# Optimization experiments

Hardware: AMD Instinct MI355X
Metric: run time of the kernel (lower is better)

## Reference

```python
import jax, jax.numpy as jnp
import numpy as np

VOCAB = 32000
DIM = 1024
DEPTH = 4
SEQ = 512
HEADS = 16
NMB = 4
MAXMEM = NMB * SEQ  # 2048
RAMP = 128
COEF = 1e-06
B = 4
DH = DIM // HEADS


def _ln(x, g, b):
    mu = jnp.mean(x, axis=-1, keepdims=True)
    v = jnp.mean((x - mu) ** 2, axis=-1, keepdims=True)
    return (x - mu) / jnp.sqrt(v + 1e-5) * g + b


def setup_inputs() -> dict:
    key = jax.random.key(0)
    ks = jax.random.split(key, 24)
    s = 0.02
    inp = {
        'tokens': jax.random.randint(ks[0], (B, SEQ), 0, VOCAB),
        'mems': jax.random.normal(ks[1], (DEPTH, B, MAXMEM, DIM), jnp.float32) * s,
        'times': jax.random.randint(ks[2], (DEPTH, MAXMEM), 0, 4096, dtype=jnp.int32),
        'token_emb': jax.random.normal(ks[3], (VOCAB, DIM), jnp.float32) * s,
        'expire_W': jax.random.normal(ks[4], (DEPTH, DIM), jnp.float32) * s,
        'expire_b': jnp.full((DEPTH,), -float(MAXMEM), jnp.float32),  # torch init constant
        'ln1_g': jnp.ones((DEPTH, DIM), jnp.float32),
        'ln1_b': jnp.zeros((DEPTH, DIM), jnp.float32),
        'Wq': jax.random.normal(ks[5], (DEPTH, DIM, DIM), jnp.float32) * s,
        'Wkv': jax.random.normal(ks[6], (DEPTH, DIM, 2 * DIM), jnp.float32) * s,
        'Wo': jax.random.normal(ks[7], (DEPTH, DIM, DIM), jnp.float32) * s,
        'bo': jnp.zeros((DEPTH, DIM), jnp.float32),
        'ln2_g': jnp.ones((DEPTH, DIM), jnp.float32),
        'ln2_b': jnp.zeros((DEPTH, DIM), jnp.float32),
        'W1': jax.random.normal(ks[8], (DEPTH, DIM, 4 * DIM), jnp.float32) * s,
        'b1': jnp.zeros((DEPTH, 4 * DIM), jnp.float32),
        'W2': jax.random.normal(ks[9], (DEPTH, 4 * DIM, DIM), jnp.float32) * s,
        'b2': jnp.zeros((DEPTH, DIM), jnp.float32),
        'logits_W': jax.random.normal(ks[10], (DIM, VOCAB), jnp.float32) * s,
        'logits_b': jnp.zeros((VOCAB,), jnp.float32),
    }
    return inp


def reference(tokens, mems, times, token_emb, expire_W, expire_b, ln1_g, ln1_b,
              Wq, Wkv, Wo, bo, ln2_g, ln2_b, W1, b1, W2, b2, logits_W, logits_b):
    n, M = SEQ, MAXMEM
    scale = DH ** -0.5
    x = token_emb[tokens]  # (B, n, DIM)
    # causal mask over concat(mem, x): query i may attend key j iff j <= i + M
    causal = jnp.triu(jnp.ones((n, M + n), bool), k=M + 1)  # True = masked
    aux = jnp.float32(0.0)
    new_mems, new_times = [], []
    tnew = jnp.arange(n - 1, -1, -1, dtype=times.dtype)
    for d in range(DEPTH):
        mem = mems[d]                       # (B, M, DIM)
        t = times[d].astype(jnp.float32)    # (M,)
        hidden = x
        # --- expire span: per-memory-slot soft retention mask ---
        exps = jax.nn.sigmoid(mem @ expire_W[d] + expire_b[d]) * M  # (B, M)
        r = exps[:, None, None, :] - t[None, None, None, :]          # (B,1,1,M)
        r = jnp.pad(r, ((0, 0), (0, 0), (0, 0), (0, n)), constant_values=1.0)
        emask = jnp.clip(r / RAMP + 1.0, 0.0, 1.0)                   # (B,1,1,M+n)
        # --- pre-norm causal attention over concat(mem, x_normed) ---
        xn = _ln(x, ln1_g[d], ln1_b[d])
        q = (xn @ Wq[d]).reshape(B, n, HEADS, DH).transpose(0, 2, 1, 3)
        ctx = jnp.concatenate([mem, xn], axis=1)                     # (B, M+n, DIM)
        kv = ctx @ Wkv[d]
        k = kv[..., :DIM].reshape(B, M + n, HEADS, DH).transpose(0, 2, 1, 3)
        v = kv[..., DIM:].reshape(B, M + n, HEADS, DH).transpose(0, 2, 1, 3)
        dots = jnp.einsum('bhid,bhjd->bhij', q, k) * scale
        dots = jnp.where(causal, -jnp.inf, dots)
        attn = jax.nn.softmax(dots, axis=-1) * emask
        out = jnp.einsum('bhij,bhjd->bhid', attn, v)
        out = out.transpose(0, 2, 1, 3).reshape(B, n, DIM)
        x = out @ Wo[d] + bo[d] + x
        # --- pre-norm FFN ---
        xn2 = _ln(x, ln2_g[d], ln2_b[d])
        x = jax.nn.gelu(xn2 @ W1[d] + b1[d], approximate=False) @ W2[d] + b2[d] + x
        aux = aux + (exps / SEQ).sum() * COEF
        # --- memory bookkeeping (detached) ---
        new_mems.append(jax.lax.stop_gradient(
            jnp.concatenate([mem, hidden], axis=1)[:, -M:]))
        new_times.append(jnp.concatenate([times[d] + n, tnew])[-M:])
    logits = x @ logits_W + logits_b
    return (logits, jnp.stack(new_mems), jnp.stack(new_times), aux)
```

## Files before the change

### kernel.cpp

```cpp
#include <hip/hip_runtime.h>
#include <cmath>

#define DIMC   1024
#define SEQC   512
#define BC     4
#define MC     2048
#define CTXC   2560
#define HEADSC 16
#define DHC    64
#define VOCABC 32000

using short8 = __attribute__((ext_vector_type(8))) short;
using f32x4  = __attribute__((ext_vector_type(4))) float;
using u16x4  = __attribute__((ext_vector_type(4))) unsigned short;
using u16x8  = __attribute__((ext_vector_type(8))) unsigned short;

__device__ __forceinline__ unsigned short f2bf(float f) {
    unsigned u = __float_as_uint(f);
    unsigned r = (u + 0x7fffu + ((u >> 16) & 1u)) >> 16;
    return (unsigned short)r;
}

__device__ __forceinline__ void glds16(const unsigned short* g, char* l) {
    __builtin_amdgcn_global_load_lds(
        (const __attribute__((address_space(1))) void*)g,
        (__attribute__((address_space(3))) void*)l, 16, 0, 0);
}

__global__ __launch_bounds__(256) void embed_kernel(const int* __restrict__ tokens,
                                                    const float* __restrict__ emb,
                                                    float* __restrict__ x) {
    int row = blockIdx.x;
    int tok = tokens[row];
    const float4 v = *(const float4*)(emb + (size_t)tok * DIMC + threadIdx.x * 4);
    *(float4*)(x + (size_t)row * DIMC + threadIdx.x * 4) = v;
}

__global__ __launch_bounds__(256) void times_init_kernel(const int* __restrict__ times,
                                                         float* __restrict__ out_times,
                                                         float* __restrict__ aux) {
    int i = blockIdx.x * 256 + threadIdx.x;
    if (i == 0) aux[0] = 0.0f;
    if (i < 4 * MC) {
        int d = i >> 11, m = i & (MC - 1);
        out_times[i] = (m < MC - SEQC) ? (float)(times[d * MC + SEQC + m] + SEQC)
                                       : (float)(MC - 1 - m);
    }
}

#define PREP_MEM 8192
#define PREP_XC  10240
#define PREP_LN  12288
#define PREP_TOT 24576
__global__ __launch_bounds__(256) void prep_kernel(
    const float* __restrict__ mem_d, const float* __restrict__ x,
    const float* __restrict__ eW, const float* __restrict__ eb,
    float* __restrict__ exps, float* __restrict__ aux,
    unsigned short* __restrict__ mem_b, float* __restrict__ out_mems_d,
    const float* __restrict__ g1, const float* __restrict__ b1v,
    unsigned short* __restrict__ xn_b,
    const float* __restrict__ Wq, const float* __restrict__ Wkv,
    const float* __restrict__ Wo, const float* __restrict__ W1,
    const float* __restrict__ W2,
    unsigned short* __restrict__ wq_t, unsigned short* __restrict__ wkv_t,
    unsigned short* __restrict__ wo_t, unsigned short* __restrict__ w1_t,
    unsigned short* __restrict__ w2_t) {
    __shared__ float sh[1056];
    const int bid = blockIdx.x, tid = threadIdx.x;
    if (bid < PREP_MEM) {
        int row = bid;
        int m = row & 2047, b = row >> 11;
        const float4 v = *(const float4*)(mem_d + (size_t)row * DIMC + tid * 4);
        const float4 w = *(const float4*)(eW + tid * 4);
        float s = v.x * w.x + v.y * w.y + v.z * w.z + v.w * w.w;
        for (int off = 32; off; off >>= 1) s += __shfl_down(s, off, 64);
        int wid = tid >> 6, lane = tid & 63;
        if (lane == 0) sh[wid] = s;
        u16x4 o = { f2bf(v.x), f2bf(v.y), f2bf(v.z), f2bf(v.w) };
        *(u16x4*)(mem_b + (size_t)row * DIMC + tid * 4) = o;
        if (m >= SEQC)
            *(float4*)(out_mems_d + ((size_t)(b * MC + m - SEQC)) * DIMC + tid * 4) = v;
        __syncthreads();
        if (tid == 0) {
            float z = sh[0] + sh[1] + sh[2] + sh[3] + eb[0];
            float e = (float)MC / (1.0f + expf(-z));
            exps[row] = e;
            atomicAdd(aux, e * (1e-6f / (float)SEQC));
        }
    } else if (bid < PREP_XC) {
        int r = bid - PREP_MEM;
        int b = r >> 9, i = r & 511;
        const float4 v = *(const float4*)(x + (size_t)r * DIMC + tid * 4);
        *(float4*)(out_mems_d + ((size_t)(b * MC + MC - SEQC + i)) * DIMC + tid * 4) = v;
    } else if (bid < PREP_LN) {
        int row = bid - PREP_XC;
        const float4 v = *(const float4*)(x + (size_t)row * DIMC + tid * 4);
        float s = v.x + v.y + v.z + v.w;
        float q = v.x * v.x + v.y * v.y + v.z * v.z + v.w * v.w;
        for (int off = 32; off; off >>= 1) {
            s += __shfl_down(s, off, 64);
            q += __shfl_down(q, off, 64);
        }
        int wid = tid >> 6, lane = tid & 63;
        if (lane == 0) { sh[wid] = s; sh[4 + wid] = q; }
        __syncthreads();
        if (tid == 0) {
            float S = sh[0] + sh[1] + sh[2] + sh[3];
            float Q = sh[4] + sh[5] + sh[6] + sh[7];
            float mu = S / DIMC;
            float var = Q / DIMC - mu * mu;
            sh[8] = mu;
            sh[9] = rsqrtf(var + 1e-5f);
        }
        __syncthreads();
        float mu = sh[8], rstd = sh[9];
        const float4 gg = *(const float4*)(g1 + tid * 4);
        const float4 bb = *(const float4*)(b1v + tid * 4);
        u16x4 o = { f2bf((v.x - mu) * rstd * gg.x + bb.x),
                    f2bf((v.y - mu) * rstd * gg.y + bb.y),
                    f2bf((v.z - mu) * rstd * gg.z + bb.z),
                    f2bf((v.w - mu) * rstd * gg.w + bb.w) };
        *(u16x4*)(xn_b + (size_t)row * DIMC + tid * 4) = o;
    } else {
        int t = bid - PREP_LN;
        const float* W; unsigned short* Wt; int K, N, tx, ty;
        if (t < 1024)      { W = Wq;  Wt = wq_t;  K = 1024; N = 1024; tx = t & 31;  ty = t >> 5; }
        else if (t < 3072) { int u = t - 1024; W = Wkv; Wt = wkv_t; K = 1024; N = 2048; tx = u & 63;  ty = u >> 6; }
        else if (t < 4096) { int u = t - 3072; W = Wo;  Wt = wo_t;  K = 1024; N = 1024; tx = u & 31;  ty = u >> 5; }
        else if (t < 8192) { int u = t - 4096; W = W1;  Wt = w1_t;  K = 1024; N = 4096; tx = u & 127; ty = u >> 7; }
        else               { int u = t - 8192; W = W2;  Wt = w2_t;  K = 4096; N = 1024; tx = u & 31;  ty = u >> 5; }
        int n0 = tx * 32, k0 = ty * 32;
        int r = tid >> 3, c = (tid & 7) * 4;
        const float4 v = *(const float4*)(W + (size_t)(k0 + r) * N + n0 + c);
        sh[r * 33 + c] = v.x; sh[r * 33 + c + 1] = v.y;
        sh[r * 33 + c + 2] = v.z; sh[r * 33 + c + 3] = v.w;
        __syncthreads();
        u16x4 o = { f2bf(sh[(c + 0) * 33 + r]), f2bf(sh[(c + 1) * 33 + r]),
                    f2bf(sh[(c + 2) * 33 + r]), f2bf(sh[(c + 3) * 33 + r]) };
        *(u16x4*)(Wt + (size_t)(n0 + r) * K + k0 + c) = o;
    }
}

__global__ __launch_bounds__(64) void compact_kernel(
    const float* __restrict__ exps, const int* __restrict__ times_d,
    int* __restrict__ cidx, float* __restrict__ em_c, int* __restrict__ cnt) {
    int b = blockIdx.x, lane = threadIdx.x;
    int c = 0;
    for (int it = 0; it < 32; ++it) {
        int j = it * 64 + lane;
        float e = exps[b * MC + j];
        float rr = (e - (float)times_d[j]) * (1.0f / 128.0f) + 1.0f;
        float em = fminf(fmaxf(rr, 0.0f), 1.0f);
        unsigned long long mk = __ballot(em > 0.0f);
        int pos = c + __popcll(mk & ((1ull << lane) - 1ull));
        if (em > 0.0f) {
            cidx[b * 2048 + pos] = j;
            em_c[b * 2048 + pos] = em;
        }
        c += __popcll(mk);
    }
    int padded = (c + 63) & ~63;
    for (int p = c + lane; p < padded; p += 64) {
        cidx[b * 2048 + p] = 0;
        em_c[b * 2048 + p] = 0.0f;
    }
    if (lane == 0) cnt[b] = padded >> 6;
}

__global__ __launch_bounds__(256) void ln_kernel(const float* __restrict__ in,
                                                 const float* __restrict__ g,
                                                 const float* __restrict__ b,
                                                 unsigned short* __restrict__ outb) {
    int row = blockIdx.x;
    int tid = threadIdx.x;
    const float4 v = *(const float4*)(in + (size_t)row * DIMC + tid * 4);
    float s = v.x + v.y + v.z + v.w;
    float q = v.x * v.x + v.y * v.y + v.z * v.z + v.w * v.w;
    for (int off = 32; off; off >>= 1) {
        s += __shfl_down(s, off, 64);
        q += __shfl_down(q, off, 64);
    }
    __shared__ float ss[4], sq[4];
    int wid = tid >> 6, lane = tid & 63;
    if (lane == 0) { ss[wid] = s; sq[wid] = q; }
    __syncthreads();
    if (tid == 0) {
        float S = ss[0] + ss[1] + ss[2] + ss[3];
        float Q = sq[0] + sq[1] + sq[2] + sq[3];
        float mu = S / DIMC;
        float var = Q / DIMC - mu * mu;
        ss[0] = mu;
        sq[0] = rsqrtf(var + 1e-5f);
    }
    __syncthreads();
    float mu = ss[0], rstd = sq[0];
    const float4 gg = *(const float4*)(g + tid * 4);
    const float4 bb = *(const float4*)(b + tid * 4);
    u16x4 o = { f2bf((v.x - mu) * rstd * gg.x + bb.x),
                f2bf((v.y - mu) * rstd * gg.y + bb.y),
                f2bf((v.z - mu) * rstd * gg.z + bb.z),
                f2bf((v.w - mu) * rstd * gg.w + bb.w) };
    *(u16x4*)(outb + (size_t)row * DIMC + tid * 4) = o;
}

__global__ __launch_bounds__(256) void wt_kernel(const float* __restrict__ W,
                                                 unsigned short* __restrict__ Wt,
                                                 int K, int N) {
    __shared__ float t[32][33];
    int tid = threadIdx.x;
    int n0 = blockIdx.x * 32, k0 = blockIdx.y * 32;
    int r = tid >> 3, c = (tid & 7) * 4;
    const float4 v = *(const float4*)(W + (size_t)(k0 + r) * N + n0 + c);
    t[r][c] = v.x; t[r][c + 1] = v.y; t[r][c + 2] = v.z; t[r][c + 3] = v.w;
    __syncthreads();
    u16x4 o = { f2bf(t[c + 0][r]), f2bf(t[c + 1][r]),
                f2bf(t[c + 2][r]), f2bf(t[c + 3][r]) };
    *(u16x4*)(Wt + (size_t)(n0 + r) * K + k0 + c) = o;
}

__global__ __launch_bounds__(256) void vt_kernel(const unsigned short* __restrict__ kvb,
                                                 unsigned short* __restrict__ vT) {
    __shared__ unsigned short t[64][72];
    int jt = blockIdx.x, dt = blockIdx.y, b = blockIdx.z;
    int j0 = MC + jt * 64;
    int tid = threadIdx.x;
    int r = tid >> 3, c = (tid & 7) * 8;
    #pragma unroll
    for (int p = 0; p < 2; ++p) {
        u16x8 v = *(const u16x8*)(kvb + ((size_t)(b * CTXC + j0 + r + p * 32)) * 2048
                                  + 1024 + dt * 64 + c);
        *(u16x8*)&t[r + p * 32][c] = v;
    }
    __syncthreads();
    #pragma unroll
    for (int p = 0; p < 2; ++p) {
        int dr = r + p * 32;
        u16x8 o = { t[c + 0][dr], t[c + 1][dr], t[c + 2][dr], t[c + 3][dr],
                    t[c + 4][dr], t[c + 5][dr], t[c + 6][dr], t[c + 7][dr] };
        *(u16x8*)(vT + ((size_t)(b * 1024 + dt * 64 + dr)) * CTXC + j0 + c) = o;
    }
}

__global__ __launch_bounds__(256) void vtc_kernel(const unsigned short* __restrict__ kvb,
                                                  const int* __restrict__ cidx,
                                                  const int* __restrict__ cnt,
                                                  unsigned short* __restrict__ vTc) {
    int ct = blockIdx.x, dt = blockIdx.y, b = blockIdx.z;
    if (ct >= cnt[b]) return;
    __shared__ unsigned short t[64][72];
    int tid = threadIdx.x;
    int r = tid >> 3, c = (tid & 7) * 8;
    #pragma unroll
    for (int p = 0; p < 2; ++p) {
        int row = cidx[b * 2048 + ct * 64 + r + p * 32];
        u16x8 v = *(const u16x8*)(kvb + ((size_t)(b * CTXC + row)) * 2048
                                  + 1024 + dt * 64 + c);
        *(u16x8*)&t[r + p * 32][c] = v;
    }
    __syncthreads();
    #pragma unroll
    for (int p = 0; p < 2; ++p) {
        int dr = r + p * 32;
        u16x8 o = { t[c + 0][dr], t[c + 1][dr], t[c + 2][dr], t[c + 3][dr],
                    t[c + 4][dr], t[c + 5][dr], t[c + 6][dr], t[c + 7][dr] };
        *(u16x8*)(vTc + ((size_t)(b * 1024 + dt * 64 + dr)) * 2048 + ct * 64 + c) = o;
    }
}

template<bool GATHER, bool BIAS, bool GELU, bool RES, int RT>
__device__ __forceinline__ void gemm_body(
    unsigned short* As, unsigned short* Bs,
    const unsigned short* __restrict__ A, const unsigned short* __restrict__ A2,
    const unsigned short* __restrict__ Wt, const float* __restrict__ bias,
    const float* __restrict__ res, float* __restrict__ Cf,
    unsigned short* __restrict__ Cb, int K, int N, int bx, int by) {
    constexpr int MF = RT / 32;
    const int tid = threadIdx.x;
    const int lane = tid & 63, wave = tid >> 6;
    const int row0 = by * RT, col0 = bx * 128;

    const int seg = tid & 3;
    const int rr0 = tid >> 2;
    const unsigned short* arow[RT / 64];
    #pragma unroll
    for (int p = 0; p < RT / 64; ++p) {
        int r = row0 + p * 64 + rr0;
        if (GATHER) {
            int b = r / CTXC, rm = r - b * CTXC;
            arow[p] = (rm < MC) ? A + ((size_t)(b * MC + rm)) * K
                                : A2 + ((size_t)(b * SEQC + rm - MC)) * K;
        } else {
            arow[p] = A + (size_t)r * K;
        }
        arow[p] += seg * 8;
    }
    const unsigned short* brow[2];
    #pragma unroll
    for (int p = 0; p < 2; ++p)
        brow[p] = Wt + (size_t)(col0 + p * 64 + rr0) * K + seg * 8;

    char* lA = (char*)As + (tid & 192) * 16;
    char* lB = (char*)Bs + (tid & 192) * 16;

    auto stage = [&](int k0, int q) {
        char* a = lA + q * (RT * 64);
        glds16(arow[0] + k0, a);
        if (RT == 128) glds16(arow[1] + k0, a + 4096);
        char* bp = lB + q * 8192;
        glds16(brow[0] + k0, bp);
        glds16(brow[1] + k0, bp + 4096);
    };

    f32x4 acc[MF][4] = {};

    const int wr = (wave >> 1) * (RT / 2), wc = (wave & 1) * 64;
    const int fr = lane & 15;
    const int k8 = (lane >> 4) * 8;

    stage(0, 0);
    __syncthreads();
    int cur = 0;
    for (int k0 = 0; k0 < K; k0 += 32) {
        if (k0 + 32 < K) stage(k0 + 32, cur ^ 1);
        const unsigned short* Ar = As + cur * (RT * 32) + (size_t)(wr + fr) * 32 + k8;
        const unsigned short* Br = Bs + cur * (128 * 32) + (size_t)(wc + fr) * 32 + k8;
        short8 a[MF], b[4];
        #pragma unroll
        for (int m = 0; m < MF; ++m) a[m] = *(const short8*)(Ar + m * 16 * 32);
        #pragma unroll
        for (int n = 0; n < 4; ++n) b[n] = *(const short8*)(Br + n * 16 * 32);
        #pragma unroll
        for (int m = 0; m < MF; ++m)
            #pragma unroll
            for (int n = 0; n < 4; ++n)
                acc[m][n] = __builtin_amdgcn_mfma_f32_16x16x32_bf16(a[m], b[n], acc[m][n], 0, 0, 0);
        __syncthreads();
        cur ^= 1;
    }

    const int orow = row0 + wr + (lane >> 4) * 4;
    const int ocol = col0 + wc + fr;
    #pragma unroll
    for (int n = 0; n < 4; ++n) {
        int c = ocol + n * 16;
        float bv = BIAS ? bias[c] : 0.0f;
        #pragma unroll
        for (int m = 0; m < MF; ++m) {
            #pragma unroll
            for (int i = 0; i < 4; ++i) {
                size_t idx = (size_t)(orow + m * 16 + i) * N + c;
                float v = acc[m][n][i] + bv;
                if (GELU) v = 0.5f * v * (1.0f + erff(v * 0.70710678118f));
                if (RES) v += res[idx];
                if (Cf) Cf[idx] = v;
                if (Cb) Cb[idx] = f2bf(v);
            }
        }
    }
}

__global__ __launch_bounds__(256) void qkv_gemm_kernel(
    const unsigned short* __restrict__ xn_b, const unsigned short* __restrict__ mem_b,
    const unsigned short* __restrict__ wq_t, const unsigned short* __restrict__ wkv_t,
    unsigned short* __restrict__ qb, unsigned short* __restrict__ kvb) {
    __shared__ unsigned short As[2 * 128 * 32];
    __shared__ unsigned short Bs[2 * 128 * 32];
    int id = blockIdx.x;
    if (id < 128) {
        gemm_body<false, false, false, false, 128>(As, Bs, xn_b, nullptr, wq_t,
            nullptr, nullptr, nullptr, qb, 1024, 1024, id & 7, id >> 3);
    } else {
        id -= 128;
        gemm_body<true, false, false, false, 128>(As, Bs, mem_b, xn_b, wkv_t,
            nullptr, nullptr, nullptr, kvb, 1024, 2048, id & 15, id >> 4);
    }
}

__global__ __launch_bounds__(256) void gemm64_kernel(
    const unsigned short* __restrict__ A, const unsigned short* __restrict__ Wt,
    const float* __restrict__ bias, const float* __restrict__ res,
    float* __restrict__ Cf, unsigned short* __restrict__ Cb, int K) {
    __shared__ unsigned short As[2 * 64 * 32];
    __shared__ unsigned short Bs[2 * 128 * 32];
    gemm_body<false, true, false, true, 64>(As, Bs, A, nullptr, Wt, bias, res,
        Cf, Cb, K, 1024, blockIdx.x, blockIdx.y);
}

__global__ __launch_bounds__(256) void ffn1_kernel(
    const unsigned short* __restrict__ A, const unsigned short* __restrict__ Wt,
    const float* __restrict__ bias, unsigned short* __restrict__ Cb) {
    __shared__ unsigned short As[2 * 128 * 32];
    __shared__ unsigned short Bs[2 * 128 * 32];
    gemm_body<false, true, true, false, 128>(As, Bs, A, nullptr, Wt, bias, nullptr,
        nullptr, Cb, 1024, 4096, blockIdx.x, blockIdx.y);
}

__global__ __launch_bounds__(256) void logits_kernel(
    const unsigned short* __restrict__ A, const unsigned short* __restrict__ Wt,
    const float* __restrict__ bias, float* __restrict__ Cf) {
    __shared__ unsigned short As[2 * 128 * 32];
    __shared__ unsigned short Bs[2 * 128 * 32];
    gemm_body<false, true, false, false, 128>(As, Bs, A, nullptr, Wt, bias, nullptr,
        Cf, nullptr, 1024, VOCABC, blockIdx.y, blockIdx.x);
}

__global__ __launch_bounds__(256) void attn_mfma_kernel(
    const unsigned short* __restrict__ qb,
    const unsigned short* __restrict__ kvb,
    const unsigned short* __restrict__ vT,
    const unsigned short* __restrict__ vTc,
    const int* __restrict__ cidx,
    const float* __restrict__ em_c,
    const int* __restrict__ cnt,
    unsigned short* __restrict__ outb) {
    __shared__ unsigned short K_s[2][64 * 64];
    __shared__ unsigned short V_s[2][64 * 64];
    __shared__ unsigned short p_s[4][16][72];
    __shared__ float em_s[64];
    const int tid = threadIdx.x;
    const int lane = tid & 63, wave = tid >> 6;
    const int qt = blockIdx.x, h = blockIdx.y, b = blockIdx.z;
    const int fr = lane & 15, g = lane >> 4;
    const int gq = qt * 64 + wave * 16;

    short8 aq[2];
    {
        const unsigned short* qp = qb + ((size_t)(b * SEQC + gq + fr)) * DIMC + h * DHC + g * 8;
        aq[0] = *(const short8*)qp;
        aq[1] = *(const short8*)(qp + 32);
    }

    const int sr = tid >> 3, ss = tid & 7;
    const int wbase = (tid & 192) * 16;

    f32x4 acc_o[4] = {};
    float m_q = -1e30f, l_q = 0.0f;

    const int nt = 33 + qt;

    auto stage12 = [&](int t, int q) {
        const int jbase = t * 64;
        #pragma unroll
        for (int p = 0; p < 2; ++p) {
            int r = sr + p * 32, sw = (ss ^ (r & 7)) * 8;
            glds16(kvb + ((size_t)(b * CTXC + jbase + r)) * 2048 + h * DHC + sw,
                   (char*)K_s[q] + wbase + p * 4096);
            if (t >= 32)
                glds16(vT + ((size_t)(b * 1024 + h * DHC + r)) * CTXC + jbase + sw,
                       (char*)V_s[q] + wbase + p * 4096);
        }
    };

    stage12(0, 0);
    __syncthreads();
    int cur = 0;
    for (int t = 0; t < nt; ++t) {
        if (t + 1 < nt) stage12(t + 1, cur ^ 1);

        f32x4 sT[4] = {};
        #pragma unroll
        for (int ks = 0; ks < 2; ++ks)
            #pragma unroll
            for (int mf = 0; mf < 4; ++mf) {
                int row = mf * 16 + fr, sg = (ks * 4 + g) ^ (row & 7);
                short8 kk = *(const short8*)((const char*)K_s[cur] + row * 128 + sg * 16);
                sT[mf] = __builtin_amdgcn_mfma_f32_16x16x32_bf16(kk, aq[ks], sT[mf], 0, 0, 0);
            }

        if (t < 32) {
            float mx = sT[0][0];
            #pragma unroll
            for (int mf = 0; mf < 4; ++mf)
                #pragma unroll
                for (int i = 0; i < 4; ++i) mx = fmaxf(mx, sT[mf][i]);
            mx *= 0.125f;
            mx = fmaxf(mx, __shfl_xor(mx, 16, 64));
            mx = fmaxf(mx, __shfl_xor(mx, 32, 64));
            float mnew = fmaxf(m_q, mx);
            float fs = __expf(m_q - mnew);
            m_q = mnew;
            float ps = 0.0f;
            #pragma unroll
            for (int mf = 0; mf < 4; ++mf)
                #pragma unroll
                for (int i = 0; i < 4; ++i)
                    ps += __expf(sT[mf][i] * 0.125f - mnew);
            ps += __shfl_xor(ps, 16, 64);
            ps += __shfl_xor(ps, 32, 64);
            l_q = l_q * fs + ps;
        } else {
            const int lt = t - 32;
            const int kq = gq + fr - lt * 64;
            float sv[4][4];
            #pragma unroll
            for (int mf = 0; mf < 4; ++mf)
                #pragma unroll
                for (int i = 0; i < 4; ++i) {
                    int kl = mf * 16 + g * 4 + i;
                    sv[mf][i] = (kl <= kq) ? sT[mf][i] * 0.125f : -1e30f;
                }
            float mx = sv[0][0];
            #pragma unroll
            for (int mf = 0; mf < 4; ++mf)
                #pragma unroll
                for (int i = 0; i < 4; ++i) mx = fmaxf(mx, sv[mf][i]);
            mx = fmaxf(mx, __shfl_xor(mx, 16, 64));
            mx = fmaxf(mx, __shfl_xor(mx, 32, 64));
            float mnew = fmaxf(m_q, mx);
            float fs = __expf(m_q - mnew);
            m_q = mnew;
            float ps = 0.0f;
            #pragma unroll
            for (int mf = 0; mf < 4; ++mf)
                #pragma unroll
                for (int i = 0; i < 4; ++i) {
                    float pe = __expf(sv[mf][i] - mnew);
                    ps += pe;
                    p_s[wave][fr][mf * 16 + g * 4 + i] = f2bf(pe);
                }
            ps += __shfl_xor(ps, 16, 64);
            ps += __shfl_xor(ps, 32, 64);
            l_q = l_q * fs + ps;
            float fsr[4];
            #pragma unroll
            for (int i = 0; i < 4; ++i) fsr[i] = __shfl(fs, g * 4 + i, 64);
            #pragma unroll
            for (int n = 0; n < 4; ++n)
                #pragma unroll
                for (int i = 0; i < 4; ++i) acc_o[n][i] *= fsr[i];
            asm volatile("s_waitcnt lgkmcnt(0)" ::: "memory");
            #pragma unroll
            for (int ks = 0; ks < 2; ++ks) {
                short8 ap = *(const short8*)&p_s[wave][fr][ks * 32 + g * 8];
                #pragma unroll
                for (int n = 0; n < 4; ++n) {
                    int row = n * 16 + fr, sg = (ks * 4 + g) ^ (row & 7);
                    short8 bv = *(const short8*)((const char*)V_s[cur] + row * 128 + sg * 16);
                    acc_o[n] = __builtin_amdgcn_mfma_f32_16x16x32_bf16(ap, bv, acc_o[n], 0, 0, 0);
                }
            }
        }
        __syncthreads();
        cur ^= 1;
    }

    const int nct = cnt[b];
    for (int ct = 0; ct < nct; ++ct) {
        __syncthreads();
        #pragma unroll
        for (int p = 0; p < 2; ++p) {
            int r = sr + p * 32, sw = (ss ^ (r & 7)) * 8;
            int row = cidx[b * 2048 + ct * 64 + r];
            glds16(kvb + ((size_t)(b * CTXC + row)) * 2048 + h * DHC + sw,
                   (char*)K_s[0] + wbase + p * 4096);
            glds16(vTc + ((size_t)(b * 1024 + h * DHC + r)) * 2048 + ct * 64 + sw,
                   (char*)V_s[0] + wbase + p * 4096);
        }
        if (tid < 64) em_s[tid] = em_c[b * 2048 + ct * 64 + tid];
        __syncthreads();
        f32x4 sT[4] = {};
        #pragma unroll
        for (int ks = 0; ks < 2; ++ks)
            #pragma unroll
            for (int mf = 0; mf < 4; ++mf) {
                int row = mf * 16 + fr, sg = (ks * 4 + g) ^ (row & 7);
                short8 kk = *(const short8*)((const char*)K_s[0] + row * 128 + sg * 16);
                sT[mf] = __builtin_amdgcn_mfma_f32_16x16x32_bf16(kk, aq[ks], sT[mf], 0, 0, 0);
            }
        #pragma unroll
        for (int mf = 0; mf < 4; ++mf)
            #pragma unroll
            for (int i = 0; i < 4; ++i) {
                int key = mf * 16 + g * 4 + i;
                float pe = __expf(sT[mf][i] * 0.125f - m_q) * em_s[key];
                p_s[wave][fr][key] = f2bf(pe);
            }
        asm volatile("s_waitcnt lgkmcnt(0)" ::: "memory");
        #pragma unroll
        for (int ks = 0; ks < 2; ++ks) {
            short8 ap = *(const short8*)&p_s[wave][fr][ks * 32 + g * 8];
            #pragma unroll
            for (int n = 0; n < 4; ++n) {
                int row = n * 16 + fr, sg = (ks * 4 + g) ^ (row & 7);
                short8 bv = *(const short8*)((const char*)V_s[0] + row * 128 + sg * 16);
                acc_o[n] = __builtin_amdgcn_mfma_f32_16x16x32_bf16(ap, bv, acc_o[n], 0, 0, 0);
            }
        }
    }

    float linv = 1.0f / l_q;
    float invr[4];
    #pragma unroll
    for (int i = 0; i < 4; ++i) invr[i] = __shfl(linv, g * 4 + i, 64);
    #pragma unroll
    for (int n = 0; n < 4; ++n) {
        #pragma unroll
        for (int i = 0; i < 4; ++i) {
            size_t idx = ((size_t)(b * SEQC + gq + g * 4 + i)) * DIMC + h * DHC + n * 16 + fr;
            outb[idx] = f2bf(acc_o[n][i] * invr[i]);
        }
    }
}

__global__ void aux_write_kernel(const float* __restrict__ aux, float* __restrict__ dst) {
    dst[0] = aux[0];
}

extern "C" void kernel_launch(void* const* d_in, const int* in_sizes, int n_in,
                              void* d_out, int out_size, void* d_ws, size_t ws_size,
                              hipStream_t stream) {
    const int*   tokens    = (const int*)d_in[0];
    const float* mems      = (const float*)d_in[1];
    const int*   times     = (const int*)d_in[2];
    const float* token_emb = (const float*)d_in[3];
    const float* expire_W  = (const float*)d_in[4];
    const float* expire_b  = (const float*)d_in[5];
    const float* ln1_g     = (const float*)d_in[6];
    const float* ln1_b     = (const float*)d_in[7];
    const float* Wq        = (const float*)d_in[8];
    const float* Wkv       = (const float*)d_in[9];
    const float* Wo        = (const float*)d_in[10];
    const float* bo        = (const float*)d_in[11];
    const float* ln2_g     = (const float*)d_in[12];
    const float* ln2_b     = (const float*)d_in[13];
    const float* W1        = (const float*)d_in[14];
    const float* b1        = (const float*)d_in[15];
    const float* W2        = (const float*)d_in[16];
    const float* b2        = (const float*)d_in[17];
    const float* logits_W  = (const float*)d_in[18];
    const float* logits_b  = (const float*)d_in[19];

    float* out = (float*)d_out;
    float* ws  = (float*)d_ws;

    float* x = ws;
    unsigned short* qb_b  = (unsigned short*)(ws + 2097152);
    unsigned short* kv_b  = (unsigned short*)(ws + 3145728);
    unsigned short* vT    = (unsigned short*)(ws + 13631488);
    unsigned short* xn_b  = (unsigned short*)(ws + 18874368);
    unsigned short* attn_b= (unsigned short*)(ws + 19922944);
    unsigned short* ffn_b = (unsigned short*)(ws + 20971520);
    unsigned short* mem_b = (unsigned short*)(ws + 25165824);
    unsigned short* x_b   = (unsigned short*)(ws + 29360128);
    unsigned short* wq_t  = (unsigned short*)(ws + 30408704);
    unsigned short* wkv_t = (unsigned short*)(ws + 30932992);
    unsigned short* wo_t  = (unsigned short*)(ws + 31981568);
    unsigned short* w1_t  = (unsigned short*)(ws + 32505856);
    unsigned short* w2_t  = (unsigned short*)(ws + 34603008);
    float* exps = ws + 36700160;
    float* aux  = ws + 36708352;
    unsigned short* vTc = (unsigned short*)(ws + 36708368);
    int*   cidx = (int*)(ws + 40902672);
    float* em_c = ws + 40910864;
    int*   cnt  = (int*)(ws + 40919056);
    unsigned short* lw_t = (unsigned short*)(ws + 2097152);

    float* out_logits = out;
    float* out_mems   = out + 65536000;
    float* out_times  = out + 99090432;

    embed_kernel<<<BC * SEQC, 256, 0, stream>>>(tokens, token_emb, x);
    times_init_kernel<<<32, 256, 0, stream>>>(times, out_times, aux);

    for (int d = 0; d < 4; ++d) {
        const float* mem_d = mems + (size_t)d * BC * MC * DIMC;
        prep_kernel<<<PREP_TOT, 256, 0, stream>>>(
            mem_d, x, expire_W + d * DIMC, expire_b + d, exps, aux,
            mem_b, out_mems + (size_t)d * BC * MC * DIMC,
            ln1_g + d * DIMC, ln1_b + d * DIMC, xn_b,
            Wq + (size_t)d * DIMC * DIMC, Wkv + (size_t)d * DIMC * 2 * DIMC,
            Wo + (size_t)d * DIMC * DIMC, W1 + (size_t)d * DIMC * 4 * DIMC,
            W2 + (size_t)d * 4 * DIMC * DIMC,
            wq_t, wkv_t, wo_t, w1_t, w2_t);
        compact_kernel<<<BC, 64, 0, stream>>>(exps, times + d * MC, cidx, em_c, cnt);
        qkv_gemm_kernel<<<1408, 256, 0, stream>>>(xn_b, mem_b, wq_t, wkv_t, qb_b, kv_b);
        vt_kernel<<<dim3(8, 16, BC), 256, 0, stream>>>(kv_b, vT);
        vtc_kernel<<<dim3(32, 16, BC), 256, 0, stream>>>(kv_b, cidx, cnt, vTc);
        attn_mfma_kernel<<<dim3(8, HEADSC, BC), 256, 0, stream>>>(
            qb_b, kv_b, vT, vTc, cidx, em_c, cnt, attn_b);
        gemm64_kernel<<<dim3(8, 32), 256, 0, stream>>>(
            attn_b, wo_t, bo + d * DIMC, x, x, nullptr, DIMC);
        ln_kernel<<<BC * SEQC, 256, 0, stream>>>(x, ln2_g + d * DIMC, ln2_b + d * DIMC, xn_b);
        ffn1_kernel<<<dim3(32, 16), 256, 0, stream>>>(xn_b, w1_t, b1 + d * 4 * DIMC, ffn_b);
        if (d < 3) {
            gemm64_kernel<<<dim3(8, 32), 256, 0, stream>>>(
                ffn_b, w2_t, b2 + d * DIMC, x, x, nullptr, 4 * DIMC);
        } else {
            gemm64_kernel<<<dim3(8, 32), 256, 0, stream>>>(
                ffn_b, w2_t, b2 + d * DIMC, x, nullptr, x_b, 4 * DIMC);
        }
    }

    wt_kernel<<<dim3(1000, 32), 256, 0, stream>>>(logits_W, lw_t, DIMC, VOCABC);
    logits_kernel<<<dim3(16, 250), 256, 0, stream>>>(x_b, lw_t, logits_b, out_logits);
    aux_write_kernel<<<1, 1, 0, stream>>>(aux, out + 99098624);
}
```

Measured before the change: 1.838 ms.

## Single-buffer GEMM LDS staging and widen attention blocks to 128 queries

The shared GEMM body drops its LDS double buffering. Each K step now loads the tile, syncs, computes and syncs again, which halves shared memory per block so more blocks can fit on a CU, but global loads no longer overlap with MFMA work. The attention kernel moves to 512-thread blocks covering 128 queries each, so every staged K/V tile is shared by twice as many waves. Each wave skips causal tiles that lie wholly past its own queries.

```diff
diff --git a/kernel.cpp b/kernel.cpp
--- a/kernel.cpp
+++ b/kernel.cpp
@@ -299,31 +299,24 @@
     for (int p = 0; p < 2; ++p)
         brow[p] = Wt + (size_t)(col0 + p * 64 + rr0) * K + seg * 8;
 
-    char* lA = (char*)As + (tid & 192) * 16;
-    char* lB = (char*)Bs + (tid & 192) * 16;
-
-    auto stage = [&](int k0, int q) {
-        char* a = lA + q * (RT * 64);
-        glds16(arow[0] + k0, a);
-        if (RT == 128) glds16(arow[1] + k0, a + 4096);
-        char* bp = lB + q * 8192;
-        glds16(brow[0] + k0, bp);
-        glds16(brow[1] + k0, bp + 4096);
-    };
+    char* lA0 = (char*)As + (tid & 192) * 16;
+    char* lB0 = (char*)Bs + (tid & 192) * 16;
+    char* lB1 = lB0 + 4096;
 
     f32x4 acc[MF][4] = {};
 
     const int wr = (wave >> 1) * (RT / 2), wc = (wave & 1) * 64;
     const int fr = lane & 15;
     const int k8 = (lane >> 4) * 8;
-
-    stage(0, 0);
-    __syncthreads();
-    int cur = 0;
+    const unsigned short* Ar = As + (size_t)(wr + fr) * 32 + k8;
+    const unsigned short* Br = Bs + (size_t)(wc + fr) * 32 + k8;
+
     for (int k0 = 0; k0 < K; k0 += 32) {
-        if (k0 + 32 < K) stage(k0 + 32, cur ^ 1);
-        const unsigned short* Ar = As + cur * (RT * 32) + (size_t)(wr + fr) * 32 + k8;
-        const unsigned short* Br = Bs + cur * (128 * 32) + (size_t)(wc + fr) * 32 + k8;
+        glds16(arow[0] + k0, lA0);
+        if (RT == 128) glds16(arow[1] + k0, lA0 + 4096);
+        glds16(brow[0] + k0, lB0);
+        glds16(brow[1] + k0, lB1);
+        __syncthreads();
         short8 a[MF], b[4];
         #pragma unroll
         for (int m = 0; m < MF; ++m) a[m] = *(const short8*)(Ar + m * 16 * 32);
@@ -335,7 +328,6 @@
             for (int n = 0; n < 4; ++n)
                 acc[m][n] = __builtin_amdgcn_mfma_f32_16x16x32_bf16(a[m], b[n], acc[m][n], 0, 0, 0);
         __syncthreads();
-        cur ^= 1;
     }
 
     const int orow = row0 + wr + (lane >> 4) * 4;
@@ -363,8 +355,8 @@
     const unsigned short* __restrict__ xn_b, const unsigned short* __restrict__ mem_b,
     const unsigned short* __restrict__ wq_t, const unsigned short* __restrict__ wkv_t,
     unsigned short* __restrict__ qb, unsigned short* __restrict__ kvb) {
-    __shared__ unsigned short As[2 * 128 * 32];
-    __shared__ unsigned short Bs[2 * 128 * 32];
+    __shared__ unsigned short As[128 * 32];
+    __shared__ unsigned short Bs[128 * 32];
     int id = blockIdx.x;
     if (id < 128) {
         gemm_body<false, false, false, false, 128>(As, Bs, xn_b, nullptr, wq_t,
@@ -380,8 +372,8 @@
     const unsigned short* __restrict__ A, const unsigned short* __restrict__ Wt,
     const float* __restrict__ bias, const float* __restrict__ res,
     float* __restrict__ Cf, unsigned short* __restrict__ Cb, int K) {
-    __shared__ unsigned short As[2 * 64 * 32];
-    __shared__ unsigned short Bs[2 * 128 * 32];
+    __shared__ unsigned short As[64 * 32];
+    __shared__ unsigned short Bs[128 * 32];
     gemm_body<false, true, false, true, 64>(As, Bs, A, nullptr, Wt, bias, res,
         Cf, Cb, K, 1024, blockIdx.x, blockIdx.y);
 }
@@ -389,8 +381,8 @@
 __global__ __launch_bounds__(256) void ffn1_kernel(
     const unsigned short* __restrict__ A, const unsigned short* __restrict__ Wt,
     const float* __restrict__ bias, unsigned short* __restrict__ Cb) {
-    __shared__ unsigned short As[2 * 128 * 32];
-    __shared__ unsigned short Bs[2 * 128 * 32];
+    __shared__ unsigned short As[128 * 32];
+    __shared__ unsigned short Bs[128 * 32];
     gemm_body<false, true, true, false, 128>(As, Bs, A, nullptr, Wt, bias, nullptr,
         nullptr, Cb, 1024, 4096, blockIdx.x, blockIdx.y);
 }
@@ -398,13 +390,13 @@
 __global__ __launch_bounds__(256) void logits_kernel(
     const unsigned short* __restrict__ A, const unsigned short* __restrict__ Wt,
     const float* __restrict__ bias, float* __restrict__ Cf) {
-    __shared__ unsigned short As[2 * 128 * 32];
-    __shared__ unsigned short Bs[2 * 128 * 32];
+    __shared__ unsigned short As[128 * 32];
+    __shared__ unsigned short Bs[128 * 32];
     gemm_body<false, true, false, false, 128>(As, Bs, A, nullptr, Wt, bias, nullptr,
         Cf, nullptr, 1024, VOCABC, blockIdx.y, blockIdx.x);
 }
 
-__global__ __launch_bounds__(256) void attn_mfma_kernel(
+__global__ __launch_bounds__(512) void attn_mfma_kernel(
     const unsigned short* __restrict__ qb,
     const unsigned short* __restrict__ kvb,
     const unsigned short* __restrict__ vT,
@@ -415,13 +407,13 @@
     unsigned short* __restrict__ outb) {
     __shared__ unsigned short K_s[2][64 * 64];
     __shared__ unsigned short V_s[2][64 * 64];
-    __shared__ unsigned short p_s[4][16][72];
+    __shared__ unsigned short p_s[8][16][72];
     __shared__ float em_s[64];
     const int tid = threadIdx.x;
     const int lane = tid & 63, wave = tid >> 6;
     const int qt = blockIdx.x, h = blockIdx.y, b = blockIdx.z;
     const int fr = lane & 15, g = lane >> 4;
-    const int gq = qt * 64 + wave * 16;
+    const int gq = qt * 128 + wave * 16;
 
     short8 aq[2];
     {
@@ -431,24 +423,22 @@
     }
 
     const int sr = tid >> 3, ss = tid & 7;
-    const int wbase = (tid & 192) * 16;
+    const int sw = (ss ^ (sr & 7)) * 8;
+    const int wbase = (tid & 448) * 16;
 
     f32x4 acc_o[4] = {};
     float m_q = -1e30f, l_q = 0.0f;
 
-    const int nt = 33 + qt;
+    const int nlt = 2 * (qt + 1);
+    const int nt = 32 + nlt;
 
     auto stage12 = [&](int t, int q) {
         const int jbase = t * 64;
-        #pragma unroll
-        for (int p = 0; p < 2; ++p) {
-            int r = sr + p * 32, sw = (ss ^ (r & 7)) * 8;
-            glds16(kvb + ((size_t)(b * CTXC + jbase + r)) * 2048 + h * DHC + sw,
-                   (char*)K_s[q] + wbase + p * 4096);
-            if (t >= 32)
-                glds16(vT + ((size_t)(b * 1024 + h * DHC + r)) * CTXC + jbase + sw,
-                       (char*)V_s[q] + wbase + p * 4096);
-        }
+        glds16(kvb + ((size_t)(b * CTXC + jbase + sr)) * 2048 + h * DHC + sw,
+               (char*)K_s[q] + wbase);
+        if (t >= 32)
+            glds16(vT + ((size_t)(b * 1024 + h * DHC + sr)) * CTXC + jbase + sw,
+                   (char*)V_s[q] + wbase);
     };
 
     stage12(0, 0);
@@ -457,86 +447,89 @@
     for (int t = 0; t < nt; ++t) {
         if (t + 1 < nt) stage12(t + 1, cur ^ 1);
 
-        f32x4 sT[4] = {};
-        #pragma unroll
-        for (int ks = 0; ks < 2; ++ks)
+        const bool live = (t < 32) || ((t - 32) * 64 <= gq + 15);
+        if (live) {
+            f32x4 sT[4] = {};
             #pragma unroll
-            for (int mf = 0; mf < 4; ++mf) {
-                int row = mf * 16 + fr, sg = (ks * 4 + g) ^ (row & 7);
-                short8 kk = *(const short8*)((const char*)K_s[cur] + row * 128 + sg * 16);
-                sT[mf] = __builtin_amdgcn_mfma_f32_16x16x32_bf16(kk, aq[ks], sT[mf], 0, 0, 0);
-            }
-
-        if (t < 32) {
-            float mx = sT[0][0];
-            #pragma unroll
-            for (int mf = 0; mf < 4; ++mf)
-                #pragma unroll
-                for (int i = 0; i < 4; ++i) mx = fmaxf(mx, sT[mf][i]);
-            mx *= 0.125f;
-            mx = fmaxf(mx, __shfl_xor(mx, 16, 64));
-            mx = fmaxf(mx, __shfl_xor(mx, 32, 64));
-            float mnew = fmaxf(m_q, mx);
-            float fs = __expf(m_q - mnew);
-            m_q = mnew;
-            float ps = 0.0f;
-            #pragma unroll
-            for (int mf = 0; mf < 4; ++mf)
-                #pragma unroll
-                for (int i = 0; i < 4; ++i)
-                    ps += __expf(sT[mf][i] * 0.125f - mnew);
-            ps += __shfl_xor(ps, 16, 64);
-            ps += __shfl_xor(ps, 32, 64);
-            l_q = l_q * fs + ps;
-        } else {
-            const int lt = t - 32;
-            const int kq = gq + fr - lt * 64;
-            float sv[4][4];
-            #pragma unroll
-            for (int mf = 0; mf < 4; ++mf)
-                #pragma unroll
-                for (int i = 0; i < 4; ++i) {
-                    int kl = mf * 16 + g * 4 + i;
-                    sv[mf][i] = (kl <= kq) ? sT[mf][i] * 0.125f : -1e30f;
+            for (int ks = 0; ks < 2; ++ks)
+                #pragma unroll
+                for (int mf = 0; mf < 4; ++mf) {
+                    int row = mf * 16 + fr, sg = (ks * 4 + g) ^ (row & 7);
+                    short8 kk = *(const short8*)((const char*)K_s[cur] + row * 128 + sg * 16);
+                    sT[mf] = __builtin_amdgcn_mfma_f32_16x16x32_bf16(kk, aq[ks], sT[mf], 0, 0, 0);
                 }
-            float mx = sv[0][0];
-            #pragma unroll
-            for (int mf = 0; mf < 4; ++mf)
-                #pragma unroll
-                for (int i = 0; i < 4; ++i) mx = fmaxf(mx, sv[mf][i]);
-            mx = fmaxf(mx, __shfl_xor(mx, 16, 64));
-            mx = fmaxf(mx, __shfl_xor(mx, 32, 64));
-            float mnew = fmaxf(m_q, mx);
-            float fs = __expf(m_q - mnew);
-            m_q = mnew;
-            float ps = 0.0f;
-            #pragma unroll
-            for (int mf = 0; mf < 4; ++mf)
-                #pragma unroll
-                for (int i = 0; i < 4; ++i) {
-                    float pe = __expf(sv[mf][i] - mnew);
-                    ps += pe;
-                    p_s[wave][fr][mf * 16 + g * 4 + i] = f2bf(pe);
-                }
-            ps += __shfl_xor(ps, 16, 64);
-            ps += __shfl_xor(ps, 32, 64);
-            l_q = l_q * fs + ps;
-            float fsr[4];
-            #pragma unroll
-            for (int i = 0; i < 4; ++i) fsr[i] = __shfl(fs, g * 4 + i, 64);
-            #pragma unroll
-            for (int n = 0; n < 4; ++n)
-                #pragma unroll
-                for (int i = 0; i < 4; ++i) acc_o[n][i] *= fsr[i];
-            asm volatile("s_waitcnt lgkmcnt(0)" ::: "memory");
-            #pragma unroll
-            for (int ks = 0; ks < 2; ++ks) {
-                short8 ap = *(const short8*)&p_s[wave][fr][ks * 32 + g * 8];
-                #pragma unroll
-                for (int n = 0; n < 4; ++n) {
-                    int row = n * 16 + fr, sg = (ks * 4 + g) ^ (row & 7);
-                    short8 bv = *(const short8*)((const char*)V_s[cur] + row * 128 + sg * 16);
-                    acc_o[n] = __builtin_amdgcn_mfma_f32_16x16x32_bf16(ap, bv, acc_o[n], 0, 0, 0);
+
+            if (t < 32) {
+                float mx = sT[0][0];
+                #pragma unroll
+                for (int mf = 0; mf < 4; ++mf)
+                    #pragma unroll
+                    for (int i = 0; i < 4; ++i) mx = fmaxf(mx, sT[mf][i]);
+                mx *= 0.125f;
+                mx = fmaxf(mx, __shfl_xor(mx, 16, 64));
+                mx = fmaxf(mx, __shfl_xor(mx, 32, 64));
+                float mnew = fmaxf(m_q, mx);
+                float fs = __expf(m_q - mnew);
+                m_q = mnew;
+                float ps = 0.0f;
+                #pragma unroll
+                for (int mf = 0; mf < 4; ++mf)
+                    #pragma unroll
+                    for (int i = 0; i < 4; ++i)
+                        ps += __expf(sT[mf][i] * 0.125f - mnew);
+                ps += __shfl_xor(ps, 16, 64);
+                ps += __shfl_xor(ps, 32, 64);
+                l_q = l_q * fs + ps;
+            } else {
+                const int lt = t - 32;
+                const int kq = gq + fr - lt * 64;
+                float sv[4][4];
+                #pragma unroll
+                for (int mf = 0; mf < 4; ++mf)
+                    #pragma unroll
+                    for (int i = 0; i < 4; ++i) {
+                        int kl = mf * 16 + g * 4 + i;
+                        sv[mf][i] = (kl <= kq) ? sT[mf][i] * 0.125f : -1e30f;
+                    }
+                float mx = sv[0][0];
+                #pragma unroll
+                for (int mf = 0; mf < 4; ++mf)
+                    #pragma unroll
+                    for (int i = 0; i < 4; ++i) mx = fmaxf(mx, sv[mf][i]);
+                mx = fmaxf(mx, __shfl_xor(mx, 16, 64));
+                mx = fmaxf(mx, __shfl_xor(mx, 32, 64));
+                float mnew = fmaxf(m_q, mx);
+                float fs = __expf(m_q - mnew);
+                m_q = mnew;
+                float ps = 0.0f;
+                #pragma unroll
+                for (int mf = 0; mf < 4; ++mf)
+                    #pragma unroll
+                    for (int i = 0; i < 4; ++i) {
+                        float pe = __expf(sv[mf][i] - mnew);
+                        ps += pe;
+                        p_s[wave][fr][mf * 16 + g * 4 + i] = f2bf(pe);
+                    }
+                ps += __shfl_xor(ps, 16, 64);
+                ps += __shfl_xor(ps, 32, 64);
+                l_q = l_q * fs + ps;
+                float fsr[4];
+                #pragma unroll
+                for (int i = 0; i < 4; ++i) fsr[i] = __shfl(fs, g * 4 + i, 64);
+                #pragma unroll
+                for (int n = 0; n < 4; ++n)
+                    #pragma unroll
+                    for (int i = 0; i < 4; ++i) acc_o[n][i] *= fsr[i];
+                asm volatile("s_waitcnt lgkmcnt(0)" ::: "memory");
+                #pragma unroll
+                for (int ks = 0; ks < 2; ++ks) {
+                    short8 ap = *(const short8*)&p_s[wave][fr][ks * 32 + g * 8];
+                    #pragma unroll
+                    for (int n = 0; n < 4; ++n) {
+                        int row = n * 16 + fr, sg = (ks * 4 + g) ^ (row & 7);
+                        short8 bv = *(const short8*)((const char*)V_s[cur] + row * 128 + sg * 16);
+                        acc_o[n] = __builtin_amdgcn_mfma_f32_16x16x32_bf16(ap, bv, acc_o[n], 0, 0, 0);
+                    }
                 }
             }
         }
@@ -547,14 +540,12 @@
     const int nct = cnt[b];
     for (int ct = 0; ct < nct; ++ct) {
         __syncthreads();
-        #pragma unroll
-        for (int p = 0; p < 2; ++p) {
-            int r = sr + p * 32, sw = (ss ^ (r & 7)) * 8;
-            int row = cidx[b * 2048 + ct * 64 + r];
+        {
+            int row = cidx[b * 2048 + ct * 64 + sr];
             glds16(kvb + ((size_t)(b * CTXC + row)) * 2048 + h * DHC + sw,
-                   (char*)K_s[0] + wbase + p * 4096);
-            glds16(vTc + ((size_t)(b * 1024 + h * DHC + r)) * 2048 + ct * 64 + sw,
-                   (char*)V_s[0] + wbase + p * 4096);
+                   (char*)K_s[0] + wbase);
+            glds16(vTc + ((size_t)(b * 1024 + h * DHC + sr)) * 2048 + ct * 64 + sw,
+                   (char*)V_s[0] + wbase);
         }
         if (tid < 64) em_s[tid] = em_c[b * 2048 + ct * 64 + tid];
         __syncthreads();
@@ -676,7 +667,7 @@
         qkv_gemm_kernel<<<1408, 256, 0, stream>>>(xn_b, mem_b, wq_t, wkv_t, qb_b, kv_b);
         vt_kernel<<<dim3(8, 16, BC), 256, 0, stream>>>(kv_b, vT);
         vtc_kernel<<<dim3(32, 16, BC), 256, 0, stream>>>(kv_b, cidx, cnt, vTc);
-        attn_mfma_kernel<<<dim3(8, HEADSC, BC), 256, 0, stream>>>(
+        attn_mfma_kernel<<<dim3(4, HEADSC, BC), 512, 0, stream>>>(
             qb_b, kv_b, vT, vTc, cidx, em_c, cnt, attn_b);
         gemm64_kernel<<<dim3(8, 32), 256, 0, stream>>>(
             attn_b, wo_t, bo + d * DIMC, x, x, nullptr, DIMC);
```

After: 1.807 ms. Within noise of the previous version (-1.7%).
